# Performance work log

Measured on AMD Instinct MI355X. Metric: run time of the kernel, lower is better.

The kernel has to match this reference:

```python
import jax, jax.numpy as jnp
import numpy as np

MARGIN = 1.0


def setup_inputs() -> dict:
    key = jax.random.key(0)
    k1, k2, k3 = jax.random.split(key, 3)
    batch, n_cards = 4096, 128
    scores = jax.random.normal(k1, (batch, n_cards), dtype=jnp.float32)
    top_mask = jax.random.randint(k2, (batch, n_cards), 0, 2).astype(jnp.int32)
    valid_mask = jax.random.randint(k3, (batch, n_cards), 0, 2).astype(jnp.int32)
    return {"scores": scores, "top_mask": top_mask, "valid_mask": valid_mask}


def reference(scores, top_mask, valid_mask):
    # top cards (anchor i) vs non-top valid cards (j)
    t = (top_mask == 1).astype(scores.dtype)                      # (B, N)
    nt = ((top_mask == 0) & (valid_mask == 1)).astype(scores.dtype)  # (B, N)
    # pair_mask[b,i,j] = 1 iff i is top and j is non-top-valid
    pair_mask = t[:, :, None] * nt[:, None, :]                    # (B, N, N)
    diff = scores[:, :, None] - scores[:, None, :]                # s_i - s_j
    hinge = jax.nn.relu(MARGIN - diff) * pair_mask
    loss = jnp.sum(hinge)
    count = jnp.sum(pair_mask)
    # original returns 0 (unnormalized) when no valid pairs exist
    return jnp.where(count > 0, loss / jnp.maximum(count, 1.0), loss)
```

## Files before the change

kernel.cpp:

```cpp
#include <hip/hip_runtime.h>

typedef float f32x2 __attribute__((ext_vector_type(2)));

__global__ __launch_bounds__(256) void prl_rows(
    const float* __restrict__ scores,
    const int* __restrict__ top_mask,
    const int* __restrict__ valid_mask,
    float* __restrict__ row_loss,
    unsigned int* __restrict__ row_cnt)
{
    __shared__ float a_sh[4][128];

    const int w    = threadIdx.x >> 6;
    const int lane = threadIdx.x & 63;
    const int row  = blockIdx.x * 4 + w;
    const size_t base = (size_t)row * 128;

    const float s0 = scores[base + lane];
    const float s1 = scores[base + lane + 64];
    const int tm0 = top_mask[base + lane],   tm1 = top_mask[base + lane + 64];
    const int vm0 = valid_mask[base + lane], vm1 = valid_mask[base + lane + 64];

    const bool top0 = (tm0 == 1), top1 = (tm1 == 1);
    const bool nt0  = (tm0 == 0) & (vm0 == 1);
    const bool nt1  = (tm1 == 0) & (vm1 == 1);

    a_sh[w][lane]      = nt0 ? (1.0f + s0) : -1e30f;
    a_sh[w][lane + 64] = nt1 ? (1.0f + s1) : -1e30f;
    __builtin_amdgcn_wave_barrier();

    f32x2 si;  si.x = s0;  si.y = s1;
    f32x2 acc; acc.x = 0.f; acc.y = 0.f;
    #pragma unroll
    for (int j = 0; j < 128; ++j) {
        const float aj = a_sh[w][j];
        f32x2 d;
        d.x = fmaxf(aj - si.x, 0.f);
        d.y = fmaxf(aj - si.y, 0.f);
        acc += d;
    }

    float lane_loss = (top0 ? acc.x : 0.f) + (top1 ? acc.y : 0.f);
    #pragma unroll
    for (int o = 32; o > 0; o >>= 1)
        lane_loss += __shfl_xor(lane_loss, o, 64);

    const unsigned long long bt0 = __ballot(top0), bt1 = __ballot(top1);
    const unsigned long long bn0 = __ballot(nt0),  bn1 = __ballot(nt1);

    if (lane == 0) {
        const unsigned t  = (unsigned)(__popcll(bt0) + __popcll(bt1));
        const unsigned nt = (unsigned)(__popcll(bn0) + __popcll(bn1));
        row_loss[row] = lane_loss;
        row_cnt[row]  = t * nt;
    }
}

__global__ __launch_bounds__(64) void prl_final(
    const float* __restrict__ row_loss,
    const unsigned int* __restrict__ row_cnt,
    float* __restrict__ out,
    int rows)
{
    const int lane = threadIdx.x;
    double l = 0.0;
    unsigned long long c = 0;
    #pragma unroll
    for (int k = 0; k < 16; ++k) {
        const int idx = lane * 4 + k * 256;
        const float4 fl = *(const float4*)(row_loss + idx);
        const uint4  cc = *(const uint4*)(row_cnt + idx);
        l += (double)((fl.x + fl.y) + (fl.z + fl.w));
        c += (unsigned long long)(cc.x + cc.y + cc.z + cc.w);
    }
    #pragma unroll
    for (int o = 32; o > 0; o >>= 1) {
        l += __shfl_xor(l, o, 64);
        c += __shfl_xor(c, o, 64);
    }
    if (lane == 0)
        out[0] = (c > 0) ? (float)(l / (double)c) : (float)l;
}

extern "C" void kernel_launch(void* const* d_in, const int* in_sizes, int n_in,
                              void* d_out, int out_size, void* d_ws, size_t ws_size,
                              hipStream_t stream) {
    const float* scores = (const float*)d_in[0];
    const int*   top    = (const int*)d_in[1];
    const int*   valid  = (const int*)d_in[2];

    const int batch   = in_sizes[0] / 128;
    const int nblocks = batch / 4;

    float*        row_loss = (float*)d_ws;
    unsigned int* row_cnt  = (unsigned int*)((char*)d_ws + (size_t)batch * sizeof(float));

    prl_rows<<<nblocks, 256, 0, stream>>>(scores, top, valid, row_loss, row_cnt);
    prl_final<<<1, 64, 0, stream>>>(row_loss, row_cnt, (float*)d_out, batch);
}
```

Measured before the change: 12.99 us.

## Fuse final reduction into row kernel via last-block atomic ticket

Merges the two kernels into one. Each block reduces its four rows in shared memory and writes a per-block partial, then takes an atomic ticket, and the last block to finish reduces all partials and writes the output. This removes the second kernel launch and its dependency gap. In exchange it adds a memset to zero the ticket, plus a __threadfence and an atomic in every block.

```diff
diff --git a/kernel.cpp b/kernel.cpp
--- a/kernel.cpp
+++ b/kernel.cpp
@@ -2,14 +2,20 @@
 
 typedef float f32x2 __attribute__((ext_vector_type(2)));
 
-__global__ __launch_bounds__(256) void prl_rows(
+__global__ __launch_bounds__(256) void prl_fused(
     const float* __restrict__ scores,
     const int* __restrict__ top_mask,
     const int* __restrict__ valid_mask,
-    float* __restrict__ row_loss,
-    unsigned int* __restrict__ row_cnt)
+    unsigned long long* __restrict__ ticket,
+    float* __restrict__ blk_loss,
+    unsigned int* __restrict__ blk_cnt,
+    float* __restrict__ out,
+    int nblocks)
 {
     __shared__ float a_sh[4][128];
+    __shared__ float wl[4];
+    __shared__ unsigned int wc[4];
+    __shared__ int is_last;
 
     const int w    = threadIdx.x >> 6;
     const int lane = threadIdx.x & 63;
@@ -51,35 +57,44 @@
     if (lane == 0) {
         const unsigned t  = (unsigned)(__popcll(bt0) + __popcll(bt1));
         const unsigned nt = (unsigned)(__popcll(bn0) + __popcll(bn1));
-        row_loss[row] = lane_loss;
-        row_cnt[row]  = t * nt;
+        wl[w] = lane_loss;
+        wc[w] = t * nt;
     }
-}
+    __syncthreads();
 
-__global__ __launch_bounds__(64) void prl_final(
-    const float* __restrict__ row_loss,
-    const unsigned int* __restrict__ row_cnt,
-    float* __restrict__ out,
-    int rows)
-{
-    const int lane = threadIdx.x;
+    if (threadIdx.x == 0) {
+        const float    bl = (wl[0] + wl[1]) + (wl[2] + wl[3]);
+        const unsigned bc = wc[0] + wc[1] + wc[2] + wc[3];
+        blk_loss[blockIdx.x] = bl;
+        blk_cnt[blockIdx.x]  = bc;
+        __threadfence();
+        const unsigned long long old = atomicAdd(ticket, 1ull);
+        is_last = (old == (unsigned long long)(nblocks - 1));
+    }
+    __syncthreads();
+    if (!is_last) return;
+
+    __threadfence();
     double l = 0.0;
     unsigned long long c = 0;
-    #pragma unroll
-    for (int k = 0; k < 16; ++k) {
-        const int idx = lane * 4 + k * 256;
-        const float4 fl = *(const float4*)(row_loss + idx);
-        const uint4  cc = *(const uint4*)(row_cnt + idx);
-        l += (double)((fl.x + fl.y) + (fl.z + fl.w));
-        c += (unsigned long long)(cc.x + cc.y + cc.z + cc.w);
+    for (int k = threadIdx.x; k < nblocks; k += 256) {
+        l += (double)((volatile const float*)blk_loss)[k];
+        c += (unsigned long long)((volatile const unsigned int*)blk_cnt)[k];
     }
     #pragma unroll
     for (int o = 32; o > 0; o >>= 1) {
         l += __shfl_xor(l, o, 64);
         c += __shfl_xor(c, o, 64);
     }
-    if (lane == 0)
-        out[0] = (c > 0) ? (float)(l / (double)c) : (float)l;
+    __shared__ double rl[4];
+    __shared__ unsigned long long rc[4];
+    if (lane == 0) { rl[w] = l; rc[w] = c; }
+    __syncthreads();
+    if (threadIdx.x == 0) {
+        const double tl = (rl[0] + rl[1]) + (rl[2] + rl[3]);
+        const unsigned long long tc = rc[0] + rc[1] + rc[2] + rc[3];
+        out[0] = (tc > 0) ? (float)(tl / (double)tc) : (float)tl;
+    }
 }
 
 extern "C" void kernel_launch(void* const* d_in, const int* in_sizes, int n_in,
@@ -92,9 +107,13 @@
     const int batch   = in_sizes[0] / 128;
     const int nblocks = batch / 4;
 
-    float*        row_loss = (float*)d_ws;
-    unsigned int* row_cnt  = (unsigned int*)((char*)d_ws + (size_t)batch * sizeof(float));
+    unsigned long long* ticket  = (unsigned long long*)d_ws;
+    float*        blk_loss = (float*)((char*)d_ws + 64);
+    unsigned int* blk_cnt  = (unsigned int*)((char*)d_ws + 64 + (size_t)nblocks * sizeof(float));
 
-    prl_rows<<<nblocks, 256, 0, stream>>>(scores, top, valid, row_loss, row_cnt);
-    prl_final<<<1, 64, 0, stream>>>(row_loss, row_cnt, (float*)d_out, batch);
+    hipMemsetAsync(d_ws, 0, 64, stream);
+
+    prl_fused<<<nblocks, 256, 0, stream>>>(scores, top, valid,
+                                           ticket, blk_loss, blk_cnt,
+                                           (float*)d_out, nblocks);
 }
```

Result: slower. 37.05 us (+185.2%).

## Fuse final reduction into row kernel via last-block atomic accumulation

Applied to the files above, without the earlier changes.

Replaces the two-kernel scheme with a single kernel. Each block reduces its rows in shared memory and adds a fixed-point loss and a packed block-count/pair-count value into global atomics, and the last block to arrive writes the result. The accumulators are reset in place, and a poison-pattern/bit-62 scheme handles uninitialized or repeated workspace contents. It also widens blocks to 8 rows with float2 loads and float2 LDS reads. This removes one kernel launch and the global round trip, at the cost of atomic contention, fixed-point rounding of the loss, and reliance on workspace state persisting across calls.

```diff
diff --git a/kernel.cpp b/kernel.cpp
--- a/kernel.cpp
+++ b/kernel.cpp
@@ -2,84 +2,99 @@
 
 typedef float f32x2 __attribute__((ext_vector_type(2)));
 
-__global__ __launch_bounds__(256) void prl_rows(
+#define ROWS_PER_BLK 8
+#define PACK_ONE (1ull << 40)
+#define CNT_MASK ((1ull << 40) - 1)
+#define POISON   0xAAAAAAAAAAAAAAAAull
+#define BIT62    (1ull << 62)
+
+__global__ __launch_bounds__(512) void prl_one(
     const float* __restrict__ scores,
     const int* __restrict__ top_mask,
     const int* __restrict__ valid_mask,
-    float* __restrict__ row_loss,
-    unsigned int* __restrict__ row_cnt)
+    unsigned long long* __restrict__ acc,
+    float* __restrict__ out,
+    int nblocks)
 {
-    __shared__ float a_sh[4][128];
+    __shared__ float a_sh[ROWS_PER_BLK][128];
+    __shared__ float wl[ROWS_PER_BLK];
+    __shared__ unsigned int wc[ROWS_PER_BLK];
 
     const int w    = threadIdx.x >> 6;
     const int lane = threadIdx.x & 63;
-    const int row  = blockIdx.x * 4 + w;
+    const int row  = blockIdx.x * ROWS_PER_BLK + w;
     const size_t base = (size_t)row * 128;
+    const int c0 = lane * 2;
 
-    const float s0 = scores[base + lane];
-    const float s1 = scores[base + lane + 64];
-    const int tm0 = top_mask[base + lane],   tm1 = top_mask[base + lane + 64];
-    const int vm0 = valid_mask[base + lane], vm1 = valid_mask[base + lane + 64];
+    const float2 s2 = *(const float2*)(scores + base + c0);
+    const int2   t2 = *(const int2*)(top_mask + base + c0);
+    const int2   v2 = *(const int2*)(valid_mask + base + c0);
 
-    const bool top0 = (tm0 == 1), top1 = (tm1 == 1);
-    const bool nt0  = (tm0 == 0) & (vm0 == 1);
-    const bool nt1  = (tm1 == 0) & (vm1 == 1);
+    const bool topA = (t2.x == 1), topB = (t2.y == 1);
+    const bool ntA  = (t2.x == 0) & (v2.x == 1);
+    const bool ntB  = (t2.y == 0) & (v2.y == 1);
 
-    a_sh[w][lane]      = nt0 ? (1.0f + s0) : -1e30f;
-    a_sh[w][lane + 64] = nt1 ? (1.0f + s1) : -1e30f;
+    float2 a2;
+    a2.x = ntA ? (1.0f + s2.x) : -1e30f;
+    a2.y = ntB ? (1.0f + s2.y) : -1e30f;
+    *(float2*)(&a_sh[w][c0]) = a2;
     __builtin_amdgcn_wave_barrier();
 
-    f32x2 si;  si.x = s0;  si.y = s1;
-    f32x2 acc; acc.x = 0.f; acc.y = 0.f;
+    f32x2 acc2; acc2.x = 0.f; acc2.y = 0.f;
     #pragma unroll
-    for (int j = 0; j < 128; ++j) {
-        const float aj = a_sh[w][j];
-        f32x2 d;
-        d.x = fmaxf(aj - si.x, 0.f);
-        d.y = fmaxf(aj - si.y, 0.f);
-        acc += d;
+    for (int j = 0; j < 128; j += 2) {
+        const float2 aj = *(const float2*)(&a_sh[w][j]);
+        f32x2 d0, d1;
+        d0.x = fmaxf(aj.x - s2.x, 0.f);
+        d0.y = fmaxf(aj.x - s2.y, 0.f);
+        d1.x = fmaxf(aj.y - s2.x, 0.f);
+        d1.y = fmaxf(aj.y - s2.y, 0.f);
+        acc2 += d0;
+        acc2 += d1;
     }
 
-    float lane_loss = (top0 ? acc.x : 0.f) + (top1 ? acc.y : 0.f);
+    float lane_loss = (topA ? acc2.x : 0.f) + (topB ? acc2.y : 0.f);
     #pragma unroll
     for (int o = 32; o > 0; o >>= 1)
         lane_loss += __shfl_xor(lane_loss, o, 64);
 
-    const unsigned long long bt0 = __ballot(top0), bt1 = __ballot(top1);
-    const unsigned long long bn0 = __ballot(nt0),  bn1 = __ballot(nt1);
+    const unsigned long long bt0 = __ballot(topA), bt1 = __ballot(topB);
+    const unsigned long long bn0 = __ballot(ntA),  bn1 = __ballot(ntB);
 
     if (lane == 0) {
         const unsigned t  = (unsigned)(__popcll(bt0) + __popcll(bt1));
         const unsigned nt = (unsigned)(__popcll(bn0) + __popcll(bn1));
-        row_loss[row] = lane_loss;
-        row_cnt[row]  = t * nt;
+        wl[w] = lane_loss;
+        wc[w] = t * nt;
     }
-}
+    __syncthreads();
 
-__global__ __launch_bounds__(64) void prl_final(
-    const float* __restrict__ row_loss,
-    const unsigned int* __restrict__ row_cnt,
-    float* __restrict__ out,
-    int rows)
-{
-    const int lane = threadIdx.x;
-    double l = 0.0;
-    unsigned long long c = 0;
-    #pragma unroll
-    for (int k = 0; k < 16; ++k) {
-        const int idx = lane * 4 + k * 256;
-        const float4 fl = *(const float4*)(row_loss + idx);
-        const uint4  cc = *(const uint4*)(row_cnt + idx);
-        l += (double)((fl.x + fl.y) + (fl.z + fl.w));
-        c += (unsigned long long)(cc.x + cc.y + cc.z + cc.w);
+    if (threadIdx.x == 0) {
+        double bl = 0.0;
+        unsigned int bc = 0;
+        #pragma unroll
+        for (int k = 0; k < ROWS_PER_BLK; ++k) { bl += (double)wl[k]; bc += wc[k]; }
+        const unsigned long long fx =
+            (unsigned long long)__double2ll_rn(bl * 16777216.0);
+
+        const unsigned long long r = atomicAdd(&acc[0], fx);
+        const unsigned long long guard = r & BIT62;
+        const unsigned long long old =
+            atomicAdd(&acc[1], PACK_ONE + (unsigned long long)bc + guard);
+
+        const unsigned long long B = (old >= (1ull << 60)) ? POISON : 0ull;
+        const unsigned long long prog = old - B;
+
+        if ((prog >> 40) == (unsigned long long)(nblocks - 1)) {
+            const unsigned long long tot = atomicAdd(&acc[0], 0ull);
+            const unsigned long long cnt = (prog & CNT_MASK) + bc;
+            const unsigned long long fxall = tot - ((B != 0ull) ? POISON : 0ull);
+            const double tl = (double)fxall * (1.0 / 16777216.0);
+            out[0] = (cnt > 0) ? (float)(tl / (double)cnt) : (float)tl;
+            atomicExch(&acc[0], tot & BIT62);
+            atomicExch(&acc[1], old & BIT62);
+        }
     }
-    #pragma unroll
-    for (int o = 32; o > 0; o >>= 1) {
-        l += __shfl_xor(l, o, 64);
-        c += __shfl_xor(c, o, 64);
-    }
-    if (lane == 0)
-        out[0] = (c > 0) ? (float)(l / (double)c) : (float)l;
 }
 
 extern "C" void kernel_launch(void* const* d_in, const int* in_sizes, int n_in,
@@ -90,11 +105,10 @@
     const int*   valid  = (const int*)d_in[2];
 
     const int batch   = in_sizes[0] / 128;
-    const int nblocks = batch / 4;
+    const int nblocks = batch / ROWS_PER_BLK;
 
-    float*        row_loss = (float*)d_ws;
-    unsigned int* row_cnt  = (unsigned int*)((char*)d_ws + (size_t)batch * sizeof(float));
+    unsigned long long* acc = (unsigned long long*)d_ws;
 
-    prl_rows<<<nblocks, 256, 0, stream>>>(scores, top, valid, row_loss, row_cnt);
-    prl_final<<<1, 64, 0, stream>>>(row_loss, row_cnt, (float*)d_out, batch);
+    prl_one<<<nblocks, 512, 0, stream>>>(scores, top, valid,
+                                         acc, (float*)d_out, nblocks);
 }
```

Result: slower. 21.95 us (+68.9%).
